# Kernel tuning notes

Hardware: AMD Instinct MI355X
Metric: run time of the kernel (lower is better)

The kernel has to match this reference:

```python
import jax, jax.numpy as jnp
import numpy as np

Na, Ns, Nb, Ne, MAXLEN, D = 16, 64, 100, 12, 20, 512
EPS = 1e-5
DELTA = 0.2
VIS_LAM = 1.0


def _make_boxes(key, shape):
    u = jax.random.uniform(key, shape + (4,), dtype=jnp.float32)
    xy = u[..., :2] * 0.7
    wh = u[..., 2:] * 0.3 + 0.01
    return jnp.concatenate([xy, xy + wh], axis=-1)  # valid xyxy boxes


def setup_inputs() -> dict:
    key = jax.random.key(0)
    k1, k2, k3, k4, k5 = jax.random.split(key, 5)
    return {
        "vis_feats": jax.random.normal(k1, (Na * Ns * Nb, D), dtype=jnp.float32),
        "word_feats": jax.random.normal(k2, (Na * Ne, D), dtype=jnp.float32),
        "boxes": _make_boxes(k3, (Na, Ns, Nb)),
        "detect_boxes": _make_boxes(k4, (Na, MAXLEN)),
        "entities_length": jax.random.randint(k5, (Na,), 0, Ne, dtype=jnp.int32),
    }


def _iou(a, b):
    # a, b: broadcastable (..., 4) xyxy. Same math as DVSA.IOU, vectorized.
    iw = jnp.minimum(a[..., 2], b[..., 2]) - jnp.maximum(a[..., 0], b[..., 0])
    ih = jnp.minimum(a[..., 3], b[..., 3]) - jnp.maximum(a[..., 1], b[..., 1])
    pos = (iw > 0) & (ih > 0)
    inter = jnp.where(pos, iw * ih, 0.0)
    a1 = (a[..., 2] - a[..., 0]) * (a[..., 3] - a[..., 1])
    a2 = (b[..., 2] - b[..., 0]) * (b[..., 3] - b[..., 1])
    denom = a1 + a2 - inter
    return jnp.where(pos, inter / jnp.where(denom > 0, denom, 1.0), 0.0)


def reference(vis_feats, word_feats, boxes, detect_boxes, entities_length):
    ar = jnp.arange(Na)
    div_vec = jnp.maximum(entities_length, 1).astype(vis_feats.dtype)          # zero2one
    word_mask = jnp.arange(Ne)[None, :] >= entities_length[:, None]            # (Na, Ne) True = padded entity

    # Ragged-masked similarity: (Na*Ns*Nb, Na*Ne)
    S_ = vis_feats @ word_feats.T
    S_ = jnp.where(word_mask.reshape(-1)[None, :], 0.0, S_)

    # Pairwise box IoU table (Na, Ns, Nb, MAXLEN) -- vectorized quadruple loop
    d_ti_n = _iou(boxes[:, :, :, None, :], detect_boxes[:, None, None, :, :])

    # --- visual consistency loss (train phase) ---
    S5 = S_.reshape(Na, Ns, Nb, Na, Ne)
    S_vis = S5[ar, :, :, ar, :]                                                # (Na, Ns, Nb, Ne) diagonal video<->caption
    sim_scr = jnp.max(S_vis, axis=2)                                           # (Na, Ns, Ne)
    maxind = jnp.argmax(S_vis, axis=2)                                         # best box per (video, seg, entity)
    flat_ind = (ar[:, None, None] * Ns + jnp.arange(Ns)[None, :, None]) * Nb + maxind
    mn = sim_scr.min(axis=1, keepdims=True)
    mx = sim_scr.max(axis=1, keepdims=True)
    sim_scr = jax.lax.stop_gradient((sim_scr - mn) / (mx - mn + EPS))[..., None]
    flat_ind = jax.lax.stop_gradient(flat_ind)

    v = vis_feats[flat_ind.reshape(-1)].reshape(Na, Ns, Ne, D)
    v = v / (jnp.linalg.norm(v, axis=3, keepdims=True) + EPS) * sim_scr
    v1 = v.transpose(0, 2, 1, 3).reshape(Na * Ne, Ns, D)
    gram = 1.0 - jnp.einsum('bsd,btd->bst', v1, v1).reshape(Na, Ne, Ns, Ns)
    eye = jnp.eye(Ns, dtype=bool)
    vis_mask = word_mask[:, :, None, None] | eye[None, None, :, :]
    gram = jnp.where(vis_mask, 0.0, gram)
    dem = jnp.maximum(jnp.count_nonzero(gram), 1).astype(gram.dtype)
    vis_loss = gram.sum() / dem

    # --- frame / margin score ---
    S = S_.reshape(Na * Ns, Nb, Na * Ne).max(axis=1).reshape(Na, Ns, Na * Ne)
    mn = S.min(axis=1, keepdims=True)
    mx = S.max(axis=1, keepdims=True)
    S = S * (S - mn) / (mx - mn + EPS)
    Sf = S.reshape(Na, Ns, Na, Ne).sum(axis=-1) / div_vec[None, None, :]        # (Na, Ns, Na)
    Sf_diag = Sf[ar, :, ar]                                                     # (Na, Ns)
    term1 = jax.nn.relu(Sf - Sf_diag.T[None, :, :] + DELTA).mean(axis=0).T      # (Na, Ns)
    term2 = jax.nn.relu(Sf - Sf_diag[:, :, None] + DELTA).mean(axis=2)          # (Na, Ns)
    frame_score = term1 + term2
    margin_loss = (frame_score.mean() + VIS_LAM * vis_loss) * 10.0

    S_sim = S_.reshape(Na * Ns, Nb, Na * Ne)
    D_sim = S_sim.max(axis=1)
    D_ind = S_sim.argmax(axis=1)
    return (D_ind, D_sim, margin_loss, d_ti_n)
```

## Files before the change

kernel.cpp:

```cpp
#include <hip/hip_runtime.h>
#include <math.h>

#define NA 16
#define NS 64
#define NB 100
#define NE 12
#define ML 20
#define DD 512
#define NC (NA*NE)
#define NR (NA*NS)
#define EPSF 1e-5f
#define DELTA_F 0.2f
#define IOU_TOTAL (NA*NS*NB*ML)
#define IOU_BLOCKS ((IOU_TOTAL + 255)/256)
#define PIT 34
#define MID_BLOCKS (NA*(NE+1))

__device__ inline void wave_minmax64(float v, float& mn, float& mx){
  mn = v; mx = v;
  #pragma unroll
  for (int off = 32; off > 0; off >>= 1){
    mn = fminf(mn, __shfl_xor(mn, off));
    mx = fmaxf(mx, __shfl_xor(mx, off));
  }
}

__device__ inline float block_sum256(float v, float* sred){
  int t = threadIdx.x;
  #pragma unroll
  for (int off = 32; off > 0; off >>= 1) v += __shfl_xor(v, off);
  if ((t & 63) == 0) sred[t >> 6] = v;
  __syncthreads();
  float tot = sred[0] + sred[1] + sred[2] + sred[3];
  __syncthreads();
  return tot;
}

template<int JC>
__device__ __forceinline__ void gemm_pass(
    const float* __restrict__ abase, const float* __restrict__ word,
    const int* __restrict__ scols, float* __restrict__ As, float* __restrict__ Bs,
    int t, int tc, int tb)
{
  float acc[7][JC];
  #pragma unroll
  for (int j = 0; j < 7; ++j)
    #pragma unroll
    for (int jc = 0; jc < JC; ++jc) acc[j][jc] = 0.f;

  for (int k0 = 0; k0 < DD; k0 += 32){
    for (int i = t; i < NB * 8; i += 256){
      int b = i >> 3, q = i & 7;
      const float4 v = *(const float4*)(abase + (size_t)b * DD + k0 + q * 4);
      float* d = &As[b * PIT + q * 4];
      *(float2*)d       = make_float2(v.x, v.y);
      *(float2*)(d + 2) = make_float2(v.z, v.w);
    }
    for (int i = t; i < JC * 16 * 8; i += 256){
      int c = i >> 3, q = i & 7;
      const float4 v = *(const float4*)(word + (size_t)scols[c] * DD + k0 + q * 4);
      float* d = &Bs[c * PIT + q * 4];
      *(float2*)d       = make_float2(v.x, v.y);
      *(float2*)(d + 2) = make_float2(v.z, v.w);
    }
    __syncthreads();
    #pragma unroll 4
    for (int kk = 0; kk < 32; kk += 2){
      float2 breg[JC], areg[7];
      #pragma unroll
      for (int jc = 0; jc < JC; ++jc)
        breg[jc] = *(const float2*)&Bs[(jc * 16 + tc) * PIT + kk];
      #pragma unroll
      for (int j = 0; j < 7; ++j){
        int b = tb * 7 + j; b = (b < NB) ? b : (NB - 1);
        areg[j] = *(const float2*)&As[b * PIT + kk];
      }
      #pragma unroll
      for (int j = 0; j < 7; ++j)
        #pragma unroll
        for (int jc = 0; jc < JC; ++jc){
          float s0 = acc[j][jc];
          s0 = fmaf(areg[j].x, breg[jc].x, s0);
          s0 = fmaf(areg[j].y, breg[jc].y, s0);
          acc[j][jc] = s0;
        }
    }
    __syncthreads();
  }
  #pragma unroll
  for (int jc = 0; jc < JC; ++jc){
    int ci = jc * 16 + tc;
    float best = -3.4e38f; int bi = 0;
    #pragma unroll
    for (int j = 0; j < 7; ++j){
      int b = tb * 7 + j;
      if (b < NB){ float v = acc[j][jc]; if (v > best){ best = v; bi = b; } }
    }
    As[ci * 16 + tb] = best;
    Bs[ci * 16 + tb] = (float)bi;
  }
}

__device__ __forceinline__ void gemm_epilogue(
    const float* __restrict__ As, const float* __restrict__ Bs,
    const int* __restrict__ scols, int base, int ncols, int kcnt,
    float* __restrict__ dsim, float* __restrict__ dind, int r, int t)
{
  __syncthreads();
  if (t < ncols){
    int gi = base + t;
    if (gi < kcnt){
      float best = -3.4e38f; int bi = 0;
      #pragma unroll
      for (int g = 0; g < 16; ++g){
        float v = As[t * 16 + g];
        if (v > best){ best = v; bi = (int)Bs[t * 16 + g]; }
      }
      int c = scols[gi];
      dsim[r * NC + c] = best;
      dind[r * NC + c] = (float)bi;
    }
  }
  __syncthreads();
}

__global__ __launch_bounds__(256) void k_main(
    const float* __restrict__ vis, const float* __restrict__ word,
    const int* __restrict__ elen, const float* __restrict__ boxes,
    const float* __restrict__ det,
    float* __restrict__ dind, float* __restrict__ dsim, float* __restrict__ dtin,
    float* __restrict__ accums, unsigned int* __restrict__ done)
{
  const int t = threadIdx.x;

  if (blockIdx.x >= NR){
    int idx = (int)(blockIdx.x - NR) * 256 + t;
    if (idx < IOU_TOTAL){
      int m = idx % ML; int t2 = idx / ML; int b = t2 % NB; int t3 = t2 / NB;
      const float4 A = *(const float4*)(boxes + (size_t)(t3 * NB + b) * 4);
      int a = t3 / NS;
      const float4 B = *(const float4*)(det + (size_t)(a * ML + m) * 4);
      float iw = fminf(A.z, B.z) - fmaxf(A.x, B.x);
      float ih = fminf(A.w, B.w) - fmaxf(A.y, B.y);
      bool pos = (iw > 0.f) && (ih > 0.f);
      float inter = pos ? iw * ih : 0.f;
      float a1 = (A.z - A.x) * (A.w - A.y);
      float a2 = (B.z - B.x) * (B.w - B.y);
      float den = a1 + a2 - inter;
      dtin[idx] = pos ? inter / (den > 0.f ? den : 1.f) : 0.f;
    }
    return;
  }

  __shared__ float As[NB * PIT];
  __shared__ float Bs[128 * PIT];
  __shared__ int   scols[NC];
  __shared__ int   s_el[NA];
  __shared__ int   s_cnt;
  const int r  = blockIdx.x;
  const int tc = t & 15;
  const int tb = t >> 4;

  if (r == 0 && t == 0){ accums[0] = 0.f; accums[1] = 0.f; done[0] = 0u; }

  if (t < NA){ int L = elen[t]; L = L < 0 ? 0 : (L > NE ? NE : L); s_el[t] = L; }
  if (t < NC){ dsim[r * NC + t] = 0.f; dind[r * NC + t] = 0.f; }
  __syncthreads();
  if (t < NC){
    int aw = t / NE, e = t - aw * NE;
    int base = 0;
    #pragma unroll
    for (int i = 0; i < NA; ++i) base += (i < aw) ? s_el[i] : 0;
    if (e < s_el[aw]) scols[base + e] = t;
  }
  if (t == 0){
    int n = 0;
    #pragma unroll
    for (int i = 0; i < NA; ++i) n += s_el[i];
    s_cnt = n;
  }
  __syncthreads();
  const int kcnt = s_cnt;
  if (t < NC && t >= kcnt) scols[t] = (kcnt > 0) ? scols[kcnt - 1] : 0;
  __syncthreads();

  const int jcnt = (kcnt + 15) >> 4;
  if (jcnt == 0) return;
  const float* abase = vis + (size_t)r * NB * DD;

  const int jc1 = (jcnt > 8) ? 8 : jcnt;
  switch (jc1){
    case 1: gemm_pass<1>(abase, word, scols, As, Bs, t, tc, tb); break;
    case 2: gemm_pass<2>(abase, word, scols, As, Bs, t, tc, tb); break;
    case 3: gemm_pass<3>(abase, word, scols, As, Bs, t, tc, tb); break;
    case 4: gemm_pass<4>(abase, word, scols, As, Bs, t, tc, tb); break;
    case 5: gemm_pass<5>(abase, word, scols, As, Bs, t, tc, tb); break;
    case 6: gemm_pass<6>(abase, word, scols, As, Bs, t, tc, tb); break;
    case 7: gemm_pass<7>(abase, word, scols, As, Bs, t, tc, tb); break;
    default: gemm_pass<8>(abase, word, scols, As, Bs, t, tc, tb); break;
  }
  gemm_epilogue(As, Bs, scols, 0, jc1 * 16, kcnt, dsim, dind, r, t);

  if (jcnt > 8){
    const int jc2 = jcnt - 8;
    switch (jc2){
      case 1: gemm_pass<1>(abase, word, scols + 128, As, Bs, t, tc, tb); break;
      case 2: gemm_pass<2>(abase, word, scols + 128, As, Bs, t, tc, tb); break;
      case 3: gemm_pass<3>(abase, word, scols + 128, As, Bs, t, tc, tb); break;
      default: gemm_pass<4>(abase, word, scols + 128, As, Bs, t, tc, tb); break;
    }
    gemm_epilogue(As, Bs, scols, 128, jc2 * 16, kcnt, dsim, dind, r, t);
  }
}

__global__ __launch_bounds__(256) void k_mid(
    const float* __restrict__ vis, const float* __restrict__ dind,
    const float* __restrict__ dsim, const int* __restrict__ elen,
    float* __restrict__ sf, float* __restrict__ accums,
    unsigned int* __restrict__ done, float* __restrict__ out)
{
  const int a = blockIdx.x, y = blockIdx.y;
  const int t = threadIdx.x, lane = t & 63, w = t >> 6;
  __shared__ float sred[4];
  __shared__ int   s_mi[NS];
  __shared__ float s_inv[NS];
  __shared__ float s_nw2[NS];
  __shared__ float s_sn[NS];
  __shared__ int   s_last;

  if (y == NE){
    for (int aw = w; aw < NA; aw += 4){
      float accv = 0.f;
      for (int e = 0; e < NE; ++e){
        int c = aw * NE + e;
        float v = dsim[(a * NS + lane) * NC + c];
        float mn, mx; wave_minmax64(v, mn, mx);
        accv += v * (v - mn) / (mx - mn + EPSF);
      }
      float dv = fmaxf((float)elen[aw], 1.f);
      sf[(a * NS + lane) * NA + aw] = accv / dv;
    }
  } else {
    const int e = y;
    if (e < elen[a]){
      if (w == 0){
        float v = dsim[(a * NS + lane) * NC + (a * NE + e)];
        float mn, mx; wave_minmax64(v, mn, mx);
        s_sn[lane] = (v - mn) / (mx - mn + EPSF);
      }
      if (t < NS) s_mi[t] = (int)dind[(size_t)(a * NS + t) * NC + (a * NE + e)];
      __syncthreads();

      for (int s = w; s < NS; s += 4){
        const float* row = vis + (size_t)((a * NS + s) * NB + s_mi[s]) * DD;
        float4 v0 = *(const float4*)(row + lane * 8);
        float4 v1 = *(const float4*)(row + lane * 8 + 4);
        float ss = v0.x*v0.x + v0.y*v0.y + v0.z*v0.z + v0.w*v0.w
                 + v1.x*v1.x + v1.y*v1.y + v1.z*v1.z + v1.w*v1.w;
        #pragma unroll
        for (int off = 32; off > 0; off >>= 1) ss += __shfl_xor(ss, off);
        if (lane == 0){
          float sn = s_sn[s];
          float d = sqrtf(ss) + EPSF;
          s_inv[s] = sn / d;
          s_nw2[s] = sn * sn * ss / (d * d);
        }
      }
      __syncthreads();

      float W0 = 0.f, W1 = 0.f;
      #pragma unroll 8
      for (int s = 0; s < NS; ++s){
        const float* row = vis + (size_t)((a * NS + s) * NB + s_mi[s]) * DD;
        float inv = s_inv[s];
        W0 = fmaf(row[t],       inv, W0);
        W1 = fmaf(row[t + 256], inv, W1);
      }
      float w2  = block_sum256(W0 * W0 + W1 * W1, sred);
      float nw2 = block_sum256((t < NS) ? s_nw2[t] : 0.f, sred);
      if (t == 0){
        float part = (float)(NS * (NS - 1)) - w2 + nw2;
        atomicAdd(&accums[0], part);
        atomicAdd(&accums[1], (float)(NS * (NS - 1)));
      }
    }
  }

  __syncthreads();
  if (t == 0){
    __threadfence();
    unsigned int old = atomicAdd(done, 1u);
    s_last = (old == (unsigned int)(MID_BLOCKS - 1)) ? 1 : 0;
  }
  __syncthreads();
  if (s_last){
    __threadfence();
    float sum = 0.f;
    for (int i = t; i < NA * NS * NA; i += 256){
      int b = i & (NA - 1);
      int a2 = i >> 10;
      float v  = sf[i];
      int s2 = (i >> 4) & (NS - 1);
      float d1 = sf[(b * NS + s2) * NA + b];
      float d2 = sf[(a2 * NS + s2) * NA + a2];
      sum += fmaxf(v - d1 + DELTA_F, 0.f) + fmaxf(v - d2 + DELTA_F, 0.f);
    }
    float tot = block_sum256(sum, sred);
    if (t == 0){
      float frame = tot / (float)(NA * NA * NS);
      float cnt = accums[1];
      float vis_loss = accums[0] / fmaxf(cnt, 1.f);
      out[0] = (frame + vis_loss) * 10.f;
    }
  }
}

extern "C" void kernel_launch(void* const* d_in, const int* in_sizes, int n_in,
                              void* d_out, int out_size, void* d_ws, size_t ws_size,
                              hipStream_t stream)
{
  const float* vis   = (const float*)d_in[0];
  const float* word  = (const float*)d_in[1];
  const float* boxes = (const float*)d_in[2];
  const float* det   = (const float*)d_in[3];
  const int*   elen  = (const int*)d_in[4];

  float* out   = (float*)d_out;
  float* dind  = out;
  float* dsim  = out + NR * NC;
  float* mloss = out + 2 * NR * NC;
  float* dtin  = mloss + 1;

  float* ws     = (float*)d_ws;
  float* sf     = ws;
  float* accums = ws + NA * NS * NA;
  unsigned int* done = (unsigned int*)(accums + 2);

  k_main<<<NR + IOU_BLOCKS, 256, 0, stream>>>(vis, word, elen, boxes, det,
                                              dind, dsim, dtin, accums, done);
  k_mid<<<dim3(NA, NE + 1), 256, 0, stream>>>(vis, dind, dsim, elen,
                                              sf, accums, done, mloss);
}
```

Baseline: 505.7 us.

## Fuse GEMM and reduction kernels into one launch with per-video completion counters

Merges the main GEMM/IoU kernel and the mid reduction kernel into a single launch. The reduction blocks sit at the end of the grid and spin on per-video atomic counters until all 64 row blocks for their video have finished. This removes the second kernel launch and lets reductions for finished videos overlap with remaining GEMM work. In exchange it adds a memset launch and a spin-wait that relies on the producer blocks being scheduled first, which can deadlock or stall if residency is limited.

```diff
diff --git a/kernel.cpp b/kernel.cpp
--- a/kernel.cpp
+++ b/kernel.cpp
@@ -14,7 +14,7 @@
 #define IOU_TOTAL (NA*NS*NB*ML)
 #define IOU_BLOCKS ((IOU_TOTAL + 255)/256)
 #define PIT 34
-#define MID_BLOCKS (NA*(NE+1))
+#define MIDB (NA*(NE+1))
 
 __device__ inline void wave_minmax64(float v, float& mn, float& mx){
   mn = v; mx = v;
@@ -124,17 +124,20 @@
   __syncthreads();
 }
 
-__global__ __launch_bounds__(256) void k_main(
+__global__ __launch_bounds__(256) void k_all(
     const float* __restrict__ vis, const float* __restrict__ word,
     const int* __restrict__ elen, const float* __restrict__ boxes,
     const float* __restrict__ det,
     float* __restrict__ dind, float* __restrict__ dsim, float* __restrict__ dtin,
-    float* __restrict__ accums, unsigned int* __restrict__ done)
+    float* __restrict__ sf, float* __restrict__ accums,
+    unsigned int* __restrict__ agent_done, unsigned int* __restrict__ mid_done,
+    float* __restrict__ out)
 {
   const int t = threadIdx.x;
-
-  if (blockIdx.x >= NR){
-    int idx = (int)(blockIdx.x - NR) * 256 + t;
+  const unsigned bx = blockIdx.x;
+
+  if (bx >= NR && bx < NR + IOU_BLOCKS){
+    int idx = (int)(bx - NR) * 256 + t;
     if (idx < IOU_TOTAL){
       int m = idx % ML; int t2 = idx / ML; int b = t2 % NB; int t3 = t2 / NB;
       const float4 A = *(const float4*)(boxes + (size_t)(t3 * NB + b) * 4);
@@ -157,76 +160,83 @@
   __shared__ int   scols[NC];
   __shared__ int   s_el[NA];
   __shared__ int   s_cnt;
-  const int r  = blockIdx.x;
-  const int tc = t & 15;
-  const int tb = t >> 4;
-
-  if (r == 0 && t == 0){ accums[0] = 0.f; accums[1] = 0.f; done[0] = 0u; }
-
-  if (t < NA){ int L = elen[t]; L = L < 0 ? 0 : (L > NE ? NE : L); s_el[t] = L; }
-  if (t < NC){ dsim[r * NC + t] = 0.f; dind[r * NC + t] = 0.f; }
-  __syncthreads();
-  if (t < NC){
-    int aw = t / NE, e = t - aw * NE;
-    int base = 0;
-    #pragma unroll
-    for (int i = 0; i < NA; ++i) base += (i < aw) ? s_el[i] : 0;
-    if (e < s_el[aw]) scols[base + e] = t;
-  }
-  if (t == 0){
-    int n = 0;
-    #pragma unroll
-    for (int i = 0; i < NA; ++i) n += s_el[i];
-    s_cnt = n;
-  }
-  __syncthreads();
-  const int kcnt = s_cnt;
-  if (t < NC && t >= kcnt) scols[t] = (kcnt > 0) ? scols[kcnt - 1] : 0;
-  __syncthreads();
-
-  const int jcnt = (kcnt + 15) >> 4;
-  if (jcnt == 0) return;
-  const float* abase = vis + (size_t)r * NB * DD;
-
-  const int jc1 = (jcnt > 8) ? 8 : jcnt;
-  switch (jc1){
-    case 1: gemm_pass<1>(abase, word, scols, As, Bs, t, tc, tb); break;
-    case 2: gemm_pass<2>(abase, word, scols, As, Bs, t, tc, tb); break;
-    case 3: gemm_pass<3>(abase, word, scols, As, Bs, t, tc, tb); break;
-    case 4: gemm_pass<4>(abase, word, scols, As, Bs, t, tc, tb); break;
-    case 5: gemm_pass<5>(abase, word, scols, As, Bs, t, tc, tb); break;
-    case 6: gemm_pass<6>(abase, word, scols, As, Bs, t, tc, tb); break;
-    case 7: gemm_pass<7>(abase, word, scols, As, Bs, t, tc, tb); break;
-    default: gemm_pass<8>(abase, word, scols, As, Bs, t, tc, tb); break;
-  }
-  gemm_epilogue(As, Bs, scols, 0, jc1 * 16, kcnt, dsim, dind, r, t);
-
-  if (jcnt > 8){
-    const int jc2 = jcnt - 8;
-    switch (jc2){
-      case 1: gemm_pass<1>(abase, word, scols + 128, As, Bs, t, tc, tb); break;
-      case 2: gemm_pass<2>(abase, word, scols + 128, As, Bs, t, tc, tb); break;
-      case 3: gemm_pass<3>(abase, word, scols + 128, As, Bs, t, tc, tb); break;
-      default: gemm_pass<4>(abase, word, scols + 128, As, Bs, t, tc, tb); break;
-    }
-    gemm_epilogue(As, Bs, scols, 128, jc2 * 16, kcnt, dsim, dind, r, t);
-  }
-}
-
-__global__ __launch_bounds__(256) void k_mid(
-    const float* __restrict__ vis, const float* __restrict__ dind,
-    const float* __restrict__ dsim, const int* __restrict__ elen,
-    float* __restrict__ sf, float* __restrict__ accums,
-    unsigned int* __restrict__ done, float* __restrict__ out)
-{
-  const int a = blockIdx.x, y = blockIdx.y;
-  const int t = threadIdx.x, lane = t & 63, w = t >> 6;
   __shared__ float sred[4];
   __shared__ int   s_mi[NS];
   __shared__ float s_inv[NS];
   __shared__ float s_nw2[NS];
   __shared__ float s_sn[NS];
   __shared__ int   s_last;
+
+  if (bx < NR){
+    const int r  = bx;
+    const int tc = t & 15;
+    const int tb = t >> 4;
+
+    if (t < NA){ int L = elen[t]; L = L < 0 ? 0 : (L > NE ? NE : L); s_el[t] = L; }
+    if (t < NC){ dsim[r * NC + t] = 0.f; dind[r * NC + t] = 0.f; }
+    __syncthreads();
+    if (t < NC){
+      int aw = t / NE, e = t - aw * NE;
+      int base = 0;
+      #pragma unroll
+      for (int i = 0; i < NA; ++i) base += (i < aw) ? s_el[i] : 0;
+      if (e < s_el[aw]) scols[base + e] = t;
+    }
+    if (t == 0){
+      int n = 0;
+      #pragma unroll
+      for (int i = 0; i < NA; ++i) n += s_el[i];
+      s_cnt = n;
+    }
+    __syncthreads();
+    const int kcnt = s_cnt;
+    if (t < NC && t >= kcnt) scols[t] = (kcnt > 0) ? scols[kcnt - 1] : 0;
+    __syncthreads();
+
+    const int jcnt = (kcnt + 15) >> 4;
+    if (jcnt > 0){
+      const float* abase = vis + (size_t)r * NB * DD;
+      const int jc1 = (jcnt > 8) ? 8 : jcnt;
+      switch (jc1){
+        case 1: gemm_pass<1>(abase, word, scols, As, Bs, t, tc, tb); break;
+        case 2: gemm_pass<2>(abase, word, scols, As, Bs, t, tc, tb); break;
+        case 3: gemm_pass<3>(abase, word, scols, As, Bs, t, tc, tb); break;
+        case 4: gemm_pass<4>(abase, word, scols, As, Bs, t, tc, tb); break;
+        case 5: gemm_pass<5>(abase, word, scols, As, Bs, t, tc, tb); break;
+        case 6: gemm_pass<6>(abase, word, scols, As, Bs, t, tc, tb); break;
+        case 7: gemm_pass<7>(abase, word, scols, As, Bs, t, tc, tb); break;
+        default: gemm_pass<8>(abase, word, scols, As, Bs, t, tc, tb); break;
+      }
+      gemm_epilogue(As, Bs, scols, 0, jc1 * 16, kcnt, dsim, dind, r, t);
+      if (jcnt > 8){
+        const int jc2 = jcnt - 8;
+        switch (jc2){
+          case 1: gemm_pass<1>(abase, word, scols + 128, As, Bs, t, tc, tb); break;
+          case 2: gemm_pass<2>(abase, word, scols + 128, As, Bs, t, tc, tb); break;
+          case 3: gemm_pass<3>(abase, word, scols + 128, As, Bs, t, tc, tb); break;
+          default: gemm_pass<4>(abase, word, scols + 128, As, Bs, t, tc, tb); break;
+        }
+        gemm_epilogue(As, Bs, scols, 128, jc2 * 16, kcnt, dsim, dind, r, t);
+      }
+    }
+    __syncthreads();
+    if (t == 0){
+      __threadfence();
+      atomicAdd(&agent_done[r >> 6], 1u);
+    }
+    return;
+  }
+
+  const int w_id = (int)(bx - NR - IOU_BLOCKS);
+  const int a = w_id / (NE + 1), y = w_id % (NE + 1);
+  const int lane = t & 63, w = t >> 6;
+
+  if (t == 0){
+    while (atomicAdd(&agent_done[a], 0u) < (unsigned)NS)
+      __builtin_amdgcn_s_sleep(8);
+    __threadfence();
+  }
+  __syncthreads();
 
   if (y == NE){
     for (int aw = w; aw < NA; aw += 4){
@@ -289,8 +299,8 @@
   __syncthreads();
   if (t == 0){
     __threadfence();
-    unsigned int old = atomicAdd(done, 1u);
-    s_last = (old == (unsigned int)(MID_BLOCKS - 1)) ? 1 : 0;
+    unsigned int old = atomicAdd(mid_done, 1u);
+    s_last = (old == (unsigned int)(MIDB - 1)) ? 1 : 0;
   }
   __syncthreads();
   if (s_last){
@@ -299,8 +309,8 @@
     for (int i = t; i < NA * NS * NA; i += 256){
       int b = i & (NA - 1);
       int a2 = i >> 10;
+      int s2 = (i >> 4) & (NS - 1);
       float v  = sf[i];
-      int s2 = (i >> 4) & (NS - 1);
       float d1 = sf[(b * NS + s2) * NA + b];
       float d2 = sf[(a2 * NS + s2) * NA + a2];
       sum += fmaxf(v - d1 + DELTA_F, 0.f) + fmaxf(v - d2 + DELTA_F, 0.f);
@@ -334,10 +344,11 @@
   float* ws     = (float*)d_ws;
   float* sf     = ws;
   float* accums = ws + NA * NS * NA;
-  unsigned int* done = (unsigned int*)(accums + 2);
-
-  k_main<<<NR + IOU_BLOCKS, 256, 0, stream>>>(vis, word, elen, boxes, det,
-                                              dind, dsim, dtin, accums, done);
-  k_mid<<<dim3(NA, NE + 1), 256, 0, stream>>>(vis, dind, dsim, elen,
-                                              sf, accums, done, mloss);
-}
+  unsigned int* agent_done = (unsigned int*)(accums + 2);
+  unsigned int* mid_done   = agent_done + NA;
+
+  hipMemsetAsync(accums, 0, (2 + NA + 1) * sizeof(float), stream);
+  k_all<<<NR + IOU_BLOCKS + MIDB, 256, 0, stream>>>(
+      vis, word, elen, boxes, det, dind, dsim, dtin,
+      sf, accums, agent_done, mid_done, mloss);
+}
```

New measurement: 545.3 us. 7.8% more time.

## Double-buffer GEMM tiles with direct global-to-LDS async loads and XOR swizzle

Applied to the files above, without the earlier changes.

Replaces the synchronous register-staged tile copy in the per-row similarity GEMM with global_load_lds direct-to-LDS loads into a double-buffered shared tile. The next k-slice is prefetched while the current one is computed, with vmcnt waits and raw barriers. Padding is dropped in favour of an XOR swizzle to avoid bank conflicts. This doubles LDS use, which may reduce occupancy, and relies on hand-coded waitcnt correctness.

```diff
diff --git a/kernel.cpp b/kernel.cpp
--- a/kernel.cpp
+++ b/kernel.cpp
@@ -13,8 +13,11 @@
 #define DELTA_F 0.2f
 #define IOU_TOTAL (NA*NS*NB*ML)
 #define IOU_BLOCKS ((IOU_TOTAL + 255)/256)
-#define PIT 34
 #define MID_BLOCKS (NA*(NE+1))
+
+#define ABUF 3328
+#define BBUF 4096
+#define TBUF (ABUF + BBUF)
 
 __device__ inline void wave_minmax64(float v, float& mn, float& mx){
   mn = v; mx = v;
@@ -36,73 +39,138 @@
   return tot;
 }
 
+__device__ __forceinline__ void wait_vmcnt(int n){
+  switch (n){
+    case 0: asm volatile("s_waitcnt vmcnt(0)" ::: "memory"); break;
+    case 1: asm volatile("s_waitcnt vmcnt(1)" ::: "memory"); break;
+    case 2: asm volatile("s_waitcnt vmcnt(2)" ::: "memory"); break;
+    case 3: asm volatile("s_waitcnt vmcnt(3)" ::: "memory"); break;
+    case 4: asm volatile("s_waitcnt vmcnt(4)" ::: "memory"); break;
+    case 5: asm volatile("s_waitcnt vmcnt(5)" ::: "memory"); break;
+    case 6: asm volatile("s_waitcnt vmcnt(6)" ::: "memory"); break;
+    case 7: asm volatile("s_waitcnt vmcnt(7)" ::: "memory"); break;
+    default: asm volatile("s_waitcnt vmcnt(8)" ::: "memory"); break;
+  }
+}
+
+#define GLOAD_LDS(gp, lp) \
+  __builtin_amdgcn_global_load_lds( \
+      (const __attribute__((address_space(1))) void*)(gp), \
+      (__attribute__((address_space(3))) void*)(lp), 16, 0, 0)
+
 template<int JC>
 __device__ __forceinline__ void gemm_pass(
     const float* __restrict__ abase, const float* __restrict__ word,
-    const int* __restrict__ scols, float* __restrict__ As, float* __restrict__ Bs,
+    const int* __restrict__ scols, float (*Tile)[TBUF],
     int t, int tc, int tb)
 {
+  constexpr int NL = 13 + 2*JC;
+  constexpr int NSLOT = (NL + 3) >> 2;
+  const int l = t & 63, w4 = t >> 6;
+  const int sub = l >> 3, q = l & 7;
+
+  int goff[NSLOT]; int ldso[NSLOT];
+  #pragma unroll
+  for (int s = 0; s < NSLOT; ++s){
+    int L = w4 + 4*s;
+    goff[s] = 0; ldso[s] = 0;
+    if (L < NL){
+      if (L < 13){
+        int rb = L*8 + sub;
+        int rbs = rb < NB ? rb : NB-1;
+        goff[s] = rbs*DD + ((q ^ (rb & 7)) << 2);
+        ldso[s] = L * 256;
+      } else {
+        int cb = (L-13)*8 + sub;
+        goff[s] = scols[cb]*DD + ((q ^ (cb & 7)) << 2);
+        ldso[s] = ABUF + (L-13) * 256;
+      }
+    }
+  }
+  const int nown = (NL - w4 + 3) >> 2;
+
   float acc[7][JC];
   #pragma unroll
   for (int j = 0; j < 7; ++j)
     #pragma unroll
     for (int jc = 0; jc < JC; ++jc) acc[j][jc] = 0.f;
 
+  #pragma unroll
+  for (int s = 0; s < NSLOT; ++s){
+    int L = w4 + 4*s;
+    if (L < NL){
+      const float* g = (L < 13 ? abase : word) + goff[s];
+      GLOAD_LDS(g, &Tile[0][ldso[s]]);
+    }
+  }
+
+  int cur = 0;
+  const int tcx = tc & 7;
   for (int k0 = 0; k0 < DD; k0 += 32){
-    for (int i = t; i < NB * 8; i += 256){
-      int b = i >> 3, q = i & 7;
-      const float4 v = *(const float4*)(abase + (size_t)b * DD + k0 + q * 4);
-      float* d = &As[b * PIT + q * 4];
-      *(float2*)d       = make_float2(v.x, v.y);
-      *(float2*)(d + 2) = make_float2(v.z, v.w);
-    }
-    for (int i = t; i < JC * 16 * 8; i += 256){
-      int c = i >> 3, q = i & 7;
-      const float4 v = *(const float4*)(word + (size_t)scols[c] * DD + k0 + q * 4);
-      float* d = &Bs[c * PIT + q * 4];
-      *(float2*)d       = make_float2(v.x, v.y);
-      *(float2*)(d + 2) = make_float2(v.z, v.w);
-    }
-    __syncthreads();
+    if (k0 + 32 < DD){
+      #pragma unroll
+      for (int s = 0; s < NSLOT; ++s){
+        int L = w4 + 4*s;
+        if (L < NL){
+          const float* g = (L < 13 ? abase : word) + goff[s] + (k0 + 32);
+          GLOAD_LDS(g, &Tile[cur^1][ldso[s]]);
+        }
+      }
+      wait_vmcnt(nown);
+    } else {
+      wait_vmcnt(0);
+    }
+    __builtin_amdgcn_sched_barrier(0);
+    __builtin_amdgcn_s_barrier();
+    __builtin_amdgcn_sched_barrier(0);
+
+    const float* As = &Tile[cur][0];
+    const float* Bs = &Tile[cur][ABUF];
     #pragma unroll 4
     for (int kk = 0; kk < 32; kk += 2){
+      const int j = kk >> 2, r2 = kk & 3;
       float2 breg[JC], areg[7];
       #pragma unroll
       for (int jc = 0; jc < JC; ++jc)
-        breg[jc] = *(const float2*)&Bs[(jc * 16 + tc) * PIT + kk];
+        breg[jc] = *(const float2*)&Bs[(jc*16 + tc)*32 + ((j ^ tcx) << 2) + r2];
       #pragma unroll
-      for (int j = 0; j < 7; ++j){
-        int b = tb * 7 + j; b = (b < NB) ? b : (NB - 1);
-        areg[j] = *(const float2*)&As[b * PIT + kk];
+      for (int jj = 0; jj < 7; ++jj){
+        int b = tb*7 + jj; b = (b < NB) ? b : (NB-1);
+        areg[jj] = *(const float2*)&As[b*32 + ((j ^ (b & 7)) << 2) + r2];
       }
       #pragma unroll
-      for (int j = 0; j < 7; ++j)
+      for (int jj = 0; jj < 7; ++jj)
         #pragma unroll
         for (int jc = 0; jc < JC; ++jc){
-          float s0 = acc[j][jc];
-          s0 = fmaf(areg[j].x, breg[jc].x, s0);
-          s0 = fmaf(areg[j].y, breg[jc].y, s0);
-          acc[j][jc] = s0;
+          float s0 = acc[jj][jc];
+          s0 = fmaf(areg[jj].x, breg[jc].x, s0);
+          s0 = fmaf(areg[jj].y, breg[jc].y, s0);
+          acc[jj][jc] = s0;
         }
     }
-    __syncthreads();
-  }
+    __builtin_amdgcn_sched_barrier(0);
+    __builtin_amdgcn_s_barrier();
+    cur ^= 1;
+  }
+
+  float* redv = &Tile[0][0];
+  float* redi = &Tile[0][ABUF];
   #pragma unroll
   for (int jc = 0; jc < JC; ++jc){
     int ci = jc * 16 + tc;
     float best = -3.4e38f; int bi = 0;
     #pragma unroll
-    for (int j = 0; j < 7; ++j){
-      int b = tb * 7 + j;
-      if (b < NB){ float v = acc[j][jc]; if (v > best){ best = v; bi = b; } }
-    }
-    As[ci * 16 + tb] = best;
-    Bs[ci * 16 + tb] = (float)bi;
+    for (int jj = 0; jj < 7; ++jj){
+      int b = tb * 7 + jj;
+      if (b < NB){ float v = acc[jj][jc]; if (v > best){ best = v; bi = b; } }
+    }
+    redv[ci * 16 + tb] = best;
+    redi[ci * 16 + tb] = (float)bi;
   }
 }
 
 __device__ __forceinline__ void gemm_epilogue(
-    const float* __restrict__ As, const float* __restrict__ Bs,
+    const float* __restrict__ redv, const float* __restrict__ redi,
     const int* __restrict__ scols, int base, int ncols, int kcnt,
     float* __restrict__ dsim, float* __restrict__ dind, int r, int t)
 {
@@ -113,8 +181,8 @@
       float best = -3.4e38f; int bi = 0;
       #pragma unroll
       for (int g = 0; g < 16; ++g){
-        float v = As[t * 16 + g];
-        if (v > best){ best = v; bi = (int)Bs[t * 16 + g]; }
+        float v = redv[t * 16 + g];
+        if (v > best){ best = v; bi = (int)redi[t * 16 + g]; }
       }
       int c = scols[gi];
       dsim[r * NC + c] = best;
@@ -152,8 +220,7 @@
     return;
   }
 
-  __shared__ float As[NB * PIT];
-  __shared__ float Bs[128 * PIT];
+  __shared__ float Tile[2][TBUF];
   __shared__ int   scols[NC];
   __shared__ int   s_el[NA];
   __shared__ int   s_cnt;
@@ -190,26 +257,25 @@
 
   const int jc1 = (jcnt > 8) ? 8 : jcnt;
   switch (jc1){
-    case 1: gemm_pass<1>(abase, word, scols, As, Bs, t, tc, tb); break;
-    case 2: gemm_pass<2>(abase, word, scols, As, Bs, t, tc, tb); break;
-    case 3: gemm_pass<3>(abase, word, scols, As, Bs, t, tc, tb); break;
-    case 4: gemm_pass<4>(abase, word, scols, As, Bs, t, tc, tb); break;
-    case 5: gemm_pass<5>(abase, word, scols, As, Bs, t, tc, tb); break;
-    case 6: gemm_pass<6>(abase, word, scols, As, Bs, t, tc, tb); break;
-    case 7: gemm_pass<7>(abase, word, scols, As, Bs, t, tc, tb); break;
-    default: gemm_pass<8>(abase, word, scols, As, Bs, t, tc, tb); break;
-  }
-  gemm_epilogue(As, Bs, scols, 0, jc1 * 16, kcnt, dsim, dind, r, t);
+    case 1: gemm_pass<1>(abase, word, scols, Tile, t, tc, tb); break;
+    case 2: gemm_pass<2>(abase, word, scols, Tile, t, tc, tb); break;
+    case 3: gemm_pass<3>(abase, word, scols, Tile, t, tc, tb); break;
+    case 4: gemm_pass<4>(abase, word, scols, Tile, t, tc, tb); break;
+    case 5: gemm_pass<5>(abase, word, scols, Tile, t, tc, tb); break;
+    case 6: gemm_pass<6>(abase, word, scols, Tile, t, tc, tb); break;
+    case 7: gemm_pass<7>(abase, word, scols, Tile, t, tc, tb); break;
+    default: gemm_pass<8>(abase, word, scols, Tile, t, tc, tb); break;
+  }
+  gemm_epilogue(&Tile[0][0], &Tile[0][ABUF], scols, 0, jc1 * 16, kcnt, dsim, dind, r, t);
 
   if (jcnt > 8){
     const int jc2 = jcnt - 8;
     switch (jc2){
-      case 1: gemm_pass<1>(abase, word, scols + 128, As, Bs, t, tc, tb); break;
-      case 2: gemm_pass<2>(abase, word, scols + 128, As, Bs, t, tc, tb); break;
-      case 3: gemm_pass<3>(abase, word, scols + 128, As, Bs, t, tc, tb); break;
-      default: gemm_pass<4>(abase, word, scols + 128, As, Bs, t, tc, tb); break;
-    }
-    gemm_epilogue(As, Bs, scols, 128, jc2 * 16, kcnt, dsim, dind, r, t);
+      case 1: gemm_pass<1>(abase, word, scols + 128, Tile, t, tc, tb); break;
+      case 2: gemm_pass<2>(abase, word, scols + 128, Tile, t, tc, tb); break;
+      default: gemm_pass<3>(abase, word, scols + 128, Tile, t, tc, tb); break;
+    }
+    gemm_epilogue(&Tile[0][0], &Tile[0][ABUF], scols, 128, jc2 * 16, kcnt, dsim, dind, r, t);
   }
 }
 
@@ -299,8 +365,8 @@
     for (int i = t; i < NA * NS * NA; i += 256){
       int b = i & (NA - 1);
       int a2 = i >> 10;
+      int s2 = (i >> 4) & (NS - 1);
       float v  = sf[i];
-      int s2 = (i >> 4) & (NS - 1);
       float d1 = sf[(b * NS + s2) * NA + b];
       float d2 = sf[(a2 * NS + s2) * NA + a2];
       sum += fmaxf(v - d1 + DELTA_F, 0.f) + fmaxf(v - d2 + DELTA_F, 0.f);
```

After: 440.1 us. 13.0% less time.
